# Kernel tuning notes

Measured on AMD Instinct MI355X. Metric: run time of the kernel, lower is better.

## Reference

```python
import jax, jax.numpy as jnp
import numpy as np

N = 20000
E = 320000
IN_DIM = 512
HID = 64
HEADS = 8
OUT_DIM = 40
NEG_SLOPE = 0.2


def glorot(key, shape):
    fan = shape[0] + shape[-1] if len(shape) > 1 else shape[-1]
    s = jnp.sqrt(6.0 / fan)
    return jax.random.uniform(key, shape, jnp.float32, -s, s)


def setup_inputs() -> dict:
    key = jax.random.key(0)
    ks = jax.random.split(key, 12)
    x = jax.random.normal(ks[0], (N, IN_DIM), jnp.float32)
    edge_index = jax.random.randint(ks[1], (2, E), 0, N, jnp.int64)
    return {
        "x": x,
        "edge_index": edge_index,
        "W1": glorot(ks[2], (IN_DIM, HEADS * HID)),
        "att1_src": glorot(ks[3], (HEADS, HID)),
        "att1_dst": glorot(ks[4], (HEADS, HID)),
        "b1": jnp.zeros((HEADS * HID,), jnp.float32),
        "W2": glorot(ks[5], (HEADS * HID, HEADS * HID)),
        "att2_src": glorot(ks[6], (HEADS, HID)),
        "att2_dst": glorot(ks[7], (HEADS, HID)),
        "b2": jnp.zeros((HEADS * HID,), jnp.float32),
        "W3": glorot(ks[8], (HEADS * HID, OUT_DIM)),
        "att3_src": glorot(ks[9], (1, OUT_DIM)),
        "att3_dst": glorot(ks[10], (1, OUT_DIM)),
        "b3": jnp.zeros((OUT_DIM,), jnp.float32),
    }


def gat_conv(x, src, dst, W, att_src, att_dst, bias, heads, out_c):
    # h: [N, H, C] transformed node features
    h = (x @ W).reshape(N, heads, out_c)
    a_src = jnp.sum(h * att_src, axis=-1)  # [N, H]
    a_dst = jnp.sum(h * att_dst, axis=-1)  # [N, H]
    # edge logits (message j=src -> i=dst), softmax grouped by dst
    logits = jax.nn.leaky_relu(a_src[src] + a_dst[dst], NEG_SLOPE)  # [Etot, H]
    seg_max = jax.ops.segment_max(logits, dst, num_segments=N)
    seg_max = jnp.where(jnp.isfinite(seg_max), seg_max, 0.0)
    ex = jnp.exp(logits - seg_max[dst])
    denom = jax.ops.segment_sum(ex, dst, num_segments=N)
    alpha = ex / (denom[dst] + 1e-16)  # [Etot, H]
    msg = h[src] * alpha[:, :, None]  # [Etot, H, C]
    out = jax.ops.segment_sum(msg, dst, num_segments=N)  # [N, H, C]
    return out.reshape(N, heads * out_c) + bias


def reference(x, edge_index, W1, att1_src, att1_dst, b1,
              W2, att2_src, att2_dst, b2,
              W3, att3_src, att3_dst, b3):
    # add self loops (PyG GATConv default)
    loops = jnp.arange(N, dtype=edge_index.dtype)
    src = jnp.concatenate([edge_index[0], loops])
    dst = jnp.concatenate([edge_index[1], loops])
    # dropout layers are identity in eval mode
    h = jax.nn.elu(gat_conv(x, src, dst, W1, att1_src, att1_dst, b1, HEADS, HID))
    h = jax.nn.elu(gat_conv(h, src, dst, W2, att2_src, att2_dst, b2, HEADS, HID))
    h = gat_conv(h, src, dst, W3, att3_src, att3_dst, b3, 1, OUT_DIM)
    return jax.nn.log_softmax(h, axis=-1)
```

## Files before the change

### kernel.cpp

```cpp
#include <hip/hip_runtime.h>
#include <math.h>

#define NN 20000
#define EE 320000
#define ETOT (EE + NN)
#define NEG 0.2f

typedef unsigned short ushortT;
typedef __attribute__((ext_vector_type(8))) short short8v;
typedef __attribute__((ext_vector_type(8))) unsigned short u16x8;
typedef __attribute__((ext_vector_type(4))) float f32x4;

__device__ __forceinline__ ushortT f2b(float f){
  unsigned u = __float_as_uint(f);
  u += 0x7FFFu + ((u >> 16) & 1u);
  return (ushortT)(u >> 16);
}
__device__ __forceinline__ float b2f(ushortT b){
  return __uint_as_float(((unsigned)b) << 16);
}

__global__ void k_cvt(const float* __restrict__ in, ushortT* __restrict__ outp, int n4){
  int i = blockIdx.x*blockDim.x + threadIdx.x;
  if(i < n4){
    float4 v = *reinterpret_cast<const float4*>(in + (size_t)i*4);
    ushort4 o;
    o.x = f2b(v.x); o.y = f2b(v.y); o.z = f2b(v.z); o.w = f2b(v.w);
    *reinterpret_cast<ushort4*>(outp + (size_t)i*4) = o;
  }
}

__global__ void k_wtrans(const float* __restrict__ W, ushortT* __restrict__ Wt){
  __shared__ float t[32][33];
  int bk = blockIdx.x*32, bn = blockIdx.y*32;
  int tx = threadIdx.x & 31, ty = threadIdx.x >> 5;
  for(int r=0;r<32;r+=8)
    t[ty+r][tx] = W[(size_t)(bk+ty+r)*512 + bn+tx];
  __syncthreads();
  for(int r=0;r<32;r+=8)
    Wt[(size_t)(bn+ty+r)*512 + bk+tx] = f2b(t[tx][ty+r]);
}

__global__ void k_wtrans3(const float* __restrict__ W3, ushortT* __restrict__ Wt3p){
  int idx = blockIdx.x*blockDim.x + threadIdx.x;
  if(idx >= 64*48*8) return;
  int kslot = idx / 384;
  int rem = idx - kslot*384;
  int n = rem >> 3;
  int jj = rem & 7;
  int k = kslot*8 + jj;
  float v = (n < 40) ? W3[(size_t)k*40 + n] : 0.f;
  Wt3p[idx] = f2b(v);
}

__global__ void k_count(const int* __restrict__ edst, int* __restrict__ counts){
  int e = blockIdx.x*blockDim.x + threadIdx.x;
  if(e < ETOT){
    int d = (e < EE) ? edst[e] : (e - EE);
    atomicAdd(&counts[d], 1);
  }
}

__global__ void k_scan(const int* __restrict__ counts, int* __restrict__ rowstart){
  __shared__ int lds[1024];
  int tid = threadIdx.x;
  int base = tid*20;
  int s = 0;
  for(int j=0;j<20;j++){ int i=base+j; if(i<NN) s += counts[i]; }
  lds[tid] = s; __syncthreads();
  for(int off=1; off<1024; off<<=1){
    int v = (tid>=off) ? lds[tid-off] : 0;
    __syncthreads();
    lds[tid] += v;
    __syncthreads();
  }
  int run = lds[tid] - s;
  for(int j=0;j<20;j++){
    int i = base+j;
    if(i <= NN){
      rowstart[i] = run;
      if(i < NN) run += counts[i];
    }
  }
}

__global__ void k_fill(const int* __restrict__ esrc, const int* __restrict__ edst,
                       const int* __restrict__ rowstart,
                       int* __restrict__ cursor, int* __restrict__ srcs,
                       int* __restrict__ edsts){
  int e = blockIdx.x*blockDim.x + threadIdx.x;
  if(e < ETOT){
    int d = (e < EE) ? edst[e] : (e - EE);
    int s = (e < EE) ? esrc[e] : (e - EE);
    int pos = rowstart[d] + atomicAdd(&cursor[d], 1);
    srcs[pos] = s;
    edsts[pos] = d;
  }
}

__global__ __launch_bounds__(256) void k_gemm_bf16(
    const ushortT* __restrict__ A, const ushortT* __restrict__ Bt,
    ushortT* __restrict__ Cb, int M)
{
  const int K = 512;
  __shared__ __align__(16) ushortT As[128*32];
  __shared__ __align__(16) ushortT Bs[128*32];
  int bm = blockIdx.x*128, bn = blockIdx.y*128;
  int tid = threadIdx.x, wave = tid>>6, lane = tid&63;
  int wm = (wave>>1)*64, wn = (wave&1)*64;
  f32x4 acc[4][4] = {};

  int l4 = lane>>2;
  int s4 = lane&3;
  int src_slot = s4 ^ (l4 & 3);
  int r16 = lane&15, kg = lane>>4;

  for(int k0=0;k0<K;k0+=32){
    #pragma unroll
    for(int c=0;c<2;c++){
      int chunk = wave*2 + c;
      int arow = bm + chunk*16 + l4; if(arow > M-1) arow = M-1;
      const ushortT* ga = A + (size_t)arow*K + k0 + src_slot*8;
      __builtin_amdgcn_global_load_lds(
          (const __attribute__((address_space(1))) void*)ga,
          (__attribute__((address_space(3))) void*)(As + chunk*16*32), 16, 0, 0);
      int brow = bn + chunk*16 + l4;
      const ushortT* gb = Bt + (size_t)brow*K + k0 + src_slot*8;
      __builtin_amdgcn_global_load_lds(
          (const __attribute__((address_space(1))) void*)gb,
          (__attribute__((address_space(3))) void*)(Bs + chunk*16*32), 16, 0, 0);
    }
    asm volatile("s_waitcnt vmcnt(0)");
    __syncthreads();

    short8v a_frag[4], b_frag[4];
    #pragma unroll
    for(int i=0;i<4;i++){
      int row = wm + i*16 + r16;
      a_frag[i] = *reinterpret_cast<const short8v*>(As + row*32 + ((kg ^ (row&3))<<3));
    }
    #pragma unroll
    for(int j=0;j<4;j++){
      int row = wn + j*16 + r16;
      b_frag[j] = *reinterpret_cast<const short8v*>(Bs + row*32 + ((kg ^ (row&3))<<3));
    }
    #pragma unroll
    for(int i=0;i<4;i++)
      #pragma unroll
      for(int j=0;j<4;j++)
        acc[i][j] = __builtin_amdgcn_mfma_f32_16x16x32_bf16(a_frag[i], b_frag[j], acc[i][j], 0, 0, 0);
    __syncthreads();
  }

  #pragma unroll
  for(int i=0;i<4;i++){
    #pragma unroll
    for(int j=0;j<4;j++){
      #pragma unroll
      for(int r=0;r<4;r++){
        int row = bm + wm + i*16 + kg*4 + r;
        int col = bn + wn + j*16 + r16;
        if(row < M) Cb[(size_t)row*512 + col] = f2b(acc[i][j][r]);
      }
    }
  }
}

__global__ __launch_bounds__(256) void k_gemm3m(const ushortT* __restrict__ A,
                                                const ushortT* __restrict__ Wt3p,
                                                ushortT* __restrict__ Cb, int M){
  const int K = 512;
  __shared__ __align__(16) ushortT As[128*32];
  __shared__ __align__(16) ushortT Bs[64*48*8];
  int bm = blockIdx.x*128;
  int tid = threadIdx.x, wave = tid>>6, lane = tid&63;

  #pragma unroll
  for(int it=0; it<12; it++){
    int o = (it*256 + tid)*8;
    *reinterpret_cast<u16x8*>(Bs + o) = *reinterpret_cast<const u16x8*>(Wt3p + o);
  }

  int l4 = lane>>2, s4 = lane&3;
  int src_slot = s4 ^ (l4 & 3);
  int r16 = lane&15, kg = lane>>4;
  f32x4 acc[2][3] = {};

  for(int k0=0;k0<K;k0+=32){
    #pragma unroll
    for(int c=0;c<2;c++){
      int chunk = wave*2 + c;
      int arow = bm + chunk*16 + l4; if(arow > M-1) arow = M-1;
      const ushortT* ga = A + (size_t)arow*K + k0 + src_slot*8;
      __builtin_amdgcn_global_load_lds(
          (const __attribute__((address_space(1))) void*)ga,
          (__attribute__((address_space(3))) void*)(As + chunk*16*32), 16, 0, 0);
    }
    asm volatile("s_waitcnt vmcnt(0)");
    __syncthreads();

    short8v a_frag[2], b_frag[3];
    #pragma unroll
    for(int i=0;i<2;i++){
      int row = wave*32 + i*16 + r16;
      a_frag[i] = *reinterpret_cast<const short8v*>(As + row*32 + ((kg ^ (row&3))<<3));
    }
    int kslot = (k0>>3) + kg;
    #pragma unroll
    for(int j=0;j<3;j++){
      b_frag[j] = *reinterpret_cast<const short8v*>(Bs + kslot*384 + (j*16 + r16)*8);
    }
    #pragma unroll
    for(int i=0;i<2;i++)
      #pragma unroll
      for(int j=0;j<3;j++)
        acc[i][j] = __builtin_amdgcn_mfma_f32_16x16x32_bf16(a_frag[i], b_frag[j], acc[i][j], 0, 0, 0);
    __syncthreads();
  }

  #pragma unroll
  for(int i=0;i<2;i++){
    #pragma unroll
    for(int j=0;j<3;j++){
      #pragma unroll
      for(int r=0;r<4;r++){
        int row = bm + wave*32 + i*16 + kg*4 + r;
        int col = j*16 + r16;
        if(row < M && col < 40) Cb[(size_t)row*40 + col] = f2b(acc[i][j][r]);
      }
    }
  }
}

__global__ void k_attn8(const ushortT* __restrict__ feat, const float* __restrict__ atts,
                        const float* __restrict__ attd, float* __restrict__ a_s,
                        float* __restrict__ a_d){
  int n = blockIdx.x*4 + (threadIdx.x>>6);
  int lane = threadIdx.x & 63;
  if(n >= NN) return;
  int c0 = lane*8;
  u16x8 v = *reinterpret_cast<const u16x8*>(feat + (size_t)n*512 + c0);
  float s1 = 0.f, s2 = 0.f;
  #pragma unroll
  for(int j=0;j<8;j++){
    float f = b2f((ushortT)v[j]);
    s1 += f*atts[c0+j];
    s2 += f*attd[c0+j];
  }
  #pragma unroll
  for(int off=1; off<8; off<<=1){
    s1 += __shfl_xor(s1, off);
    s2 += __shfl_xor(s2, off);
  }
  if((lane&7) == 0){
    int head = lane>>3;
    a_s[n*8+head] = s1;
    a_d[n*8+head] = s2;
  }
}

__global__ void k_attn1b(const ushortT* __restrict__ feat, const float* __restrict__ atts,
                         const float* __restrict__ attd, float* __restrict__ a_s,
                         float* __restrict__ a_d){
  int n = blockIdx.x*4 + (threadIdx.x>>6);
  int lane = threadIdx.x & 63;
  if(n >= NN) return;
  float s1 = 0.f, s2 = 0.f;
  if(lane < 40){
    float v = b2f(feat[(size_t)n*40 + lane]);
    s1 = v*atts[lane];
    s2 = v*attd[lane];
  }
  for(int off=32; off; off>>=1){
    s1 += __shfl_xor(s1, off);
    s2 += __shfl_xor(s2, off);
  }
  if(lane == 0){ a_s[n] = s1; a_d[n] = s2; }
}

__global__ void k_edge_pre(const int* __restrict__ srcs, const int* __restrict__ edsts,
                           const float* __restrict__ a_s, const float* __restrict__ a_d,
                           unsigned* __restrict__ rec){
  int pos = blockIdx.x*blockDim.x + threadIdx.x;
  if(pos >= ETOT) return;
  int s = srcs[pos], d = edsts[pos];
  float4 s0 = *reinterpret_cast<const float4*>(a_s + ((size_t)s<<3));
  float4 s1 = *reinterpret_cast<const float4*>(a_s + ((size_t)s<<3) + 4);
  float4 d0 = *reinterpret_cast<const float4*>(a_d + ((size_t)d<<3));
  float4 d1 = *reinterpret_cast<const float4*>(a_d + ((size_t)d<<3) + 4);
  float l[8] = { s0.x+d0.x, s0.y+d0.y, s0.z+d0.z, s0.w+d0.w,
                 s1.x+d1.x, s1.y+d1.y, s1.z+d1.z, s1.w+d1.w };
  unsigned sh = ((unsigned)s) << 16;
  #pragma unroll
  for(int h=0;h<8;h++){
    float al = __expf(fmaxf(l[h], NEG*l[h]));
    rec[(size_t)h*ETOT + pos] = sh | (unsigned)f2b(al);
  }
}

__global__ __launch_bounds__(512) void k_agg512(const ushortT* __restrict__ feat,
    const unsigned* __restrict__ rec, const int* __restrict__ rowstart,
    const float* __restrict__ bias, ushortT* __restrict__ outb){
  int slice = blockIdx.x & 7;
  int lane  = threadIdx.x & 63;
  int ds = lane>>3, cg = lane&7;
  int d = (blockIdx.x>>3)*64 + (int)(threadIdx.x>>6)*8 + ds;
  bool dok = d < NN;
  int p  = dok ? rowstart[d]   : 0;
  int p1 = dok ? rowstart[d+1] : 0;
  const unsigned* plane = rec + (size_t)slice*ETOT;
  unsigned cbase = ((unsigned)slice<<6) + ((unsigned)cg<<3);
  float acc[8] = {0.f,0.f,0.f,0.f,0.f,0.f,0.f,0.f};
  float dsum = 0.f;

  for(; p+4 <= p1; p += 4){
    unsigned r0 = plane[p];
    unsigned r1 = plane[p+1];
    unsigned r2 = plane[p+2];
    unsigned r3 = plane[p+3];
    u16x8 v0 = *reinterpret_cast<const u16x8*>(feat + ((r0>>16<<9) + cbase));
    u16x8 v1 = *reinterpret_cast<const u16x8*>(feat + ((r1>>16<<9) + cbase));
    u16x8 v2 = *reinterpret_cast<const u16x8*>(feat + ((r2>>16<<9) + cbase));
    u16x8 v3 = *reinterpret_cast<const u16x8*>(feat + ((r3>>16<<9) + cbase));
    float al0 = b2f((ushortT)(r0 & 0xffffu));
    float al1 = b2f((ushortT)(r1 & 0xffffu));
    float al2 = b2f((ushortT)(r2 & 0xffffu));
    float al3 = b2f((ushortT)(r3 & 0xffffu));
    dsum += al0 + al1 + al2 + al3;
    #pragma unroll
    for(int j=0;j<8;j++) acc[j] += al0*b2f((ushortT)v0[j]);
    #pragma unroll
    for(int j=0;j<8;j++) acc[j] += al1*b2f((ushortT)v1[j]);
    #pragma unroll
    for(int j=0;j<8;j++) acc[j] += al2*b2f((ushortT)v2[j]);
    #pragma unroll
    for(int j=0;j<8;j++) acc[j] += al3*b2f((ushortT)v3[j]);
  }
  while(__any(p < p1)){
    bool valid = p < p1;
    int pc = valid ? p : 0;
    unsigned r = plane[pc];
    float al = valid ? b2f((ushortT)(r & 0xffffu)) : 0.f;
    u16x8 v = *reinterpret_cast<const u16x8*>(feat + ((r>>16<<9) + cbase));
    dsum += al;
    #pragma unroll
    for(int j=0;j<8;j++) acc[j] += al*b2f((ushortT)v[j]);
    p++;
  }

  if(dok){
    float invd = 1.f/(dsum + 1e-16f);
    u16x8 ov;
    #pragma unroll
    for(int j=0;j<8;j++){
      float o = acc[j]*invd + bias[cbase+j];
      o = (o > 0.f) ? o : (__expf(o) - 1.f);
      ov[j] = f2b(o);
    }
    *reinterpret_cast<u16x8*>(outb + (size_t)d*512 + cbase) = ov;
  }
}

__global__ void k_agg_l3(const ushortT* __restrict__ feat,
    const float* __restrict__ a_s, const float* __restrict__ a_d,
    const int* __restrict__ rowstart, const int* __restrict__ srcs,
    const float* __restrict__ bias, float* __restrict__ outp){
  int d = blockIdx.x;
  int lane = threadIdx.x;
  bool act = lane < 40;
  int li = act ? lane : 0;
  float ad_v = a_d[d];
  float acc = 0.f, dsum = 0.f;
  int p0 = rowstart[d], p1 = rowstart[d+1];
  int p = p0;
  for(; p+4 <= p1; p += 4){
    int s0_ = srcs[p], s1_ = srcs[p+1], s2_ = srcs[p+2], s3_ = srcs[p+3];
    float l0 = a_s[s0_] + ad_v, l1 = a_s[s1_] + ad_v;
    float l2 = a_s[s2_] + ad_v, l3 = a_s[s3_] + ad_v;
    float v0 = b2f(feat[(size_t)s0_*40 + li]);
    float v1 = b2f(feat[(size_t)s1_*40 + li]);
    float v2 = b2f(feat[(size_t)s2_*40 + li]);
    float v3 = b2f(feat[(size_t)s3_*40 + li]);
    float al0 = __expf(fmaxf(l0, NEG*l0));
    float al1 = __expf(fmaxf(l1, NEG*l1));
    float al2 = __expf(fmaxf(l2, NEG*l2));
    float al3 = __expf(fmaxf(l3, NEG*l3));
    dsum += al0 + al1 + al2 + al3;
    acc += al0*v0 + al1*v1 + al2*v2 + al3*v3;
  }
  for(; p<p1; p++){
    int s_ = srcs[p];
    float l = a_s[s_] + ad_v;
    float al = __expf(fmaxf(l, NEG*l));
    dsum += al;
    acc += al*b2f(feat[(size_t)s_*40 + li]);
  }
  float invd = 1.f/(dsum + 1e-16f);
  float o = act ? (acc*invd + bias[lane]) : -1e30f;
  float m = o;
  for(int off=32; off; off>>=1) m = fmaxf(m, __shfl_xor(m, off));
  float e_ = act ? expf(o - m) : 0.f;
  float ssum = e_;
  for(int off=32; off; off>>=1) ssum += __shfl_xor(ssum, off);
  if(act) outp[(size_t)d*40 + lane] = o - m - logf(ssum);
}

extern "C" void kernel_launch(void* const* d_in, const int* in_sizes, int n_in,
                              void* d_out, int out_size, void* d_ws, size_t ws_size,
                              hipStream_t stream){
  const float* x   = (const float*)d_in[0];
  const int*   ei  = (const int*)d_in[1];
  const int*   esrc = ei;
  const int*   edst = ei + EE;
  const float* W1  = (const float*)d_in[2];
  const float* as1 = (const float*)d_in[3];
  const float* ad1 = (const float*)d_in[4];
  const float* b1  = (const float*)d_in[5];
  const float* W2  = (const float*)d_in[6];
  const float* as2 = (const float*)d_in[7];
  const float* ad2 = (const float*)d_in[8];
  const float* b2  = (const float*)d_in[9];
  const float* W3  = (const float*)d_in[10];
  const float* as3 = (const float*)d_in[11];
  const float* ad3 = (const float*)d_in[12];
  const float* b3  = (const float*)d_in[13];
  float* out = (float*)d_out;

  char* w = (char*)d_ws;
  size_t off = 0;
  auto alloc = [&](size_t bytes)->char*{
    char* p = w + off;
    off = (off + bytes + 255) & ~(size_t)255;
    return p;
  };
  ushortT*  xb   = (ushortT*)alloc((size_t)NN*512*2);
  ushortT*  fA   = (ushortT*)alloc((size_t)NN*512*2);
  ushortT*  fB   = (ushortT*)alloc((size_t)NN*512*2);
  ushortT*  h3b  = (ushortT*)alloc((size_t)NN*40*2);
  ushortT*  Wt1  = (ushortT*)alloc((size_t)512*512*2);
  ushortT*  Wt2  = (ushortT*)alloc((size_t)512*512*2);
  ushortT*  Wt3p = (ushortT*)alloc((size_t)64*48*8*2);
  float*    a_s  = (float*)alloc((size_t)NN*8*4);
  float*    a_d  = (float*)alloc((size_t)NN*8*4);
  unsigned* rec  = (unsigned*)alloc((size_t)8*ETOT*4);
  int* rowstart  = (int*)alloc((size_t)(NN+1)*4);
  int* cursor    = (int*)alloc((size_t)NN*4);
  int* counts    = (int*)alloc((size_t)NN*4);
  int* srcs      = (int*)alloc((size_t)ETOT*4);
  int* edsts     = (int*)alloc((size_t)ETOT*4);

  k_cvt<<<(NN*512/4 + 255)/256, 256, 0, stream>>>(x, xb, NN*512/4);
  dim3 wt_grid(16, 16);
  k_wtrans<<<wt_grid, 256, 0, stream>>>(W1, Wt1);
  k_wtrans<<<wt_grid, 256, 0, stream>>>(W2, Wt2);
  k_wtrans3<<<(64*48*8 + 255)/256, 256, 0, stream>>>(W3, Wt3p);

  hipMemsetAsync(counts, 0, (size_t)NN*4, stream);
  hipMemsetAsync(cursor, 0, (size_t)NN*4, stream);
  k_count<<<(ETOT+255)/256, 256, 0, stream>>>(edst, counts);
  k_scan<<<1, 1024, 0, stream>>>(counts, rowstart);
  k_fill<<<(ETOT+255)/256, 256, 0, stream>>>(esrc, edst, rowstart, cursor, srcs, edsts);

  dim3 mgrid((NN+127)/128, 4);
  int edge_blocks = (ETOT + 255)/256;
  int agg_blocks  = ((NN + 63)/64)*8;

  k_gemm_bf16<<<mgrid, 256, 0, stream>>>(xb, Wt1, fA, NN);
  k_attn8<<<(NN+3)/4, 256, 0, stream>>>(fA, as1, ad1, a_s, a_d);
  k_edge_pre<<<edge_blocks, 256, 0, stream>>>(srcs, edsts, a_s, a_d, rec);
  k_agg512<<<agg_blocks, 512, 0, stream>>>(fA, rec, rowstart, b1, fB);

  k_gemm_bf16<<<mgrid, 256, 0, stream>>>(fB, Wt2, fA, NN);
  k_attn8<<<(NN+3)/4, 256, 0, stream>>>(fA, as2, ad2, a_s, a_d);
  k_edge_pre<<<edge_blocks, 256, 0, stream>>>(srcs, edsts, a_s, a_d, rec);
  k_agg512<<<agg_blocks, 512, 0, stream>>>(fA, rec, rowstart, b2, fB);

  k_gemm3m<<<(NN+127)/128, 256, 0, stream>>>(fB, Wt3p, h3b, NN);
  k_attn1b<<<(NN+3)/4, 256, 0, stream>>>(h3b, as3, ad3, a_s, a_d);
  k_agg_l3<<<NN, 64, 0, stream>>>(h3b, a_s, a_d, rowstart, srcs, b3, out);
}
```

Measured before the change: 240.1 us.

## Fuse prep kernels into one launch and double GEMM K-tile to 64

Merges the x conversion and the three weight transpose/convert kernels into a single launch, with block ranges selecting the role, so three kernel launches disappear. Separately, the bf16 GEMM now stages 64-wide K tiles with an 8-way XOR swizzle and runs two MFMA sub-steps per tile, which halves the number of barrier/wait iterations. LDS use doubles to 32KB per block, which may reduce occupancy.

Result: faster. 233.4 us (-2.8%).

```diff
diff --git a/kernel.cpp b/kernel.cpp
--- a/kernel.cpp
+++ b/kernel.cpp
@@ -20,37 +20,41 @@
   return __uint_as_float(((unsigned)b) << 16);
 }
 
-__global__ void k_cvt(const float* __restrict__ in, ushortT* __restrict__ outp, int n4){
-  int i = blockIdx.x*blockDim.x + threadIdx.x;
-  if(i < n4){
-    float4 v = *reinterpret_cast<const float4*>(in + (size_t)i*4);
+__global__ void k_prep(const float* __restrict__ x, ushortT* __restrict__ xb,
+                       const float* __restrict__ W1, ushortT* __restrict__ Wt1,
+                       const float* __restrict__ W2, ushortT* __restrict__ Wt2,
+                       const float* __restrict__ W3, ushortT* __restrict__ Wt3p){
+  int b = blockIdx.x;
+  if(b < 10000){
+    int i = b*256 + threadIdx.x;
+    float4 v = *reinterpret_cast<const float4*>(x + (size_t)i*4);
     ushort4 o;
     o.x = f2b(v.x); o.y = f2b(v.y); o.z = f2b(v.z); o.w = f2b(v.w);
-    *reinterpret_cast<ushort4*>(outp + (size_t)i*4) = o;
-  }
-}
-
-__global__ void k_wtrans(const float* __restrict__ W, ushortT* __restrict__ Wt){
-  __shared__ float t[32][33];
-  int bk = blockIdx.x*32, bn = blockIdx.y*32;
-  int tx = threadIdx.x & 31, ty = threadIdx.x >> 5;
-  for(int r=0;r<32;r+=8)
-    t[ty+r][tx] = W[(size_t)(bk+ty+r)*512 + bn+tx];
-  __syncthreads();
-  for(int r=0;r<32;r+=8)
-    Wt[(size_t)(bn+ty+r)*512 + bk+tx] = f2b(t[tx][ty+r]);
-}
-
-__global__ void k_wtrans3(const float* __restrict__ W3, ushortT* __restrict__ Wt3p){
-  int idx = blockIdx.x*blockDim.x + threadIdx.x;
-  if(idx >= 64*48*8) return;
-  int kslot = idx / 384;
-  int rem = idx - kslot*384;
-  int n = rem >> 3;
-  int jj = rem & 7;
-  int k = kslot*8 + jj;
-  float v = (n < 40) ? W3[(size_t)k*40 + n] : 0.f;
-  Wt3p[idx] = f2b(v);
+    *reinterpret_cast<ushort4*>(xb + (size_t)i*4) = o;
+  } else if(b < 10512){
+    const float* W = (b < 10256) ? W1 : W2;
+    ushortT* Wt    = (b < 10256) ? Wt1 : Wt2;
+    int bb = (b < 10256) ? (b - 10000) : (b - 10256);
+    __shared__ float t[32][33];
+    int bk = (bb & 15)*32, bn = (bb >> 4)*32;
+    int tx = threadIdx.x & 31, ty = threadIdx.x >> 5;
+    for(int r=0;r<32;r+=8)
+      t[ty+r][tx] = W[(size_t)(bk+ty+r)*512 + bn+tx];
+    __syncthreads();
+    for(int r=0;r<32;r+=8)
+      Wt[(size_t)(bn+ty+r)*512 + bk+tx] = f2b(t[tx][ty+r]);
+  } else {
+    int idx = (b - 10512)*256 + threadIdx.x;
+    if(idx < 64*48*8){
+      int kslot = idx / 384;
+      int rem = idx - kslot*384;
+      int n = rem >> 3;
+      int jj = rem & 7;
+      int k = kslot*8 + jj;
+      float v = (n < 40) ? W3[(size_t)k*40 + n] : 0.f;
+      Wt3p[idx] = f2b(v);
+    }
+  }
 }
 
 __global__ void k_count(const int* __restrict__ edst, int* __restrict__ counts){
@@ -103,52 +107,55 @@
     ushortT* __restrict__ Cb, int M)
 {
   const int K = 512;
-  __shared__ __align__(16) ushortT As[128*32];
-  __shared__ __align__(16) ushortT Bs[128*32];
+  __shared__ __align__(16) ushortT As[128*64];
+  __shared__ __align__(16) ushortT Bs[128*64];
   int bm = blockIdx.x*128, bn = blockIdx.y*128;
   int tid = threadIdx.x, wave = tid>>6, lane = tid&63;
   int wm = (wave>>1)*64, wn = (wave&1)*64;
   f32x4 acc[4][4] = {};
 
-  int l4 = lane>>2;
-  int s4 = lane&3;
-  int src_slot = s4 ^ (l4 & 3);
+  int l8 = lane>>3;
+  int s8 = lane&7;
+  int src_slot = s8 ^ l8;
   int r16 = lane&15, kg = lane>>4;
 
-  for(int k0=0;k0<K;k0+=32){
-    #pragma unroll
-    for(int c=0;c<2;c++){
-      int chunk = wave*2 + c;
-      int arow = bm + chunk*16 + l4; if(arow > M-1) arow = M-1;
+  for(int k0=0;k0<K;k0+=64){
+    #pragma unroll
+    for(int c=0;c<4;c++){
+      int chunk = wave*4 + c;
+      int arow = bm + chunk*8 + l8; if(arow > M-1) arow = M-1;
       const ushortT* ga = A + (size_t)arow*K + k0 + src_slot*8;
       __builtin_amdgcn_global_load_lds(
           (const __attribute__((address_space(1))) void*)ga,
-          (__attribute__((address_space(3))) void*)(As + chunk*16*32), 16, 0, 0);
-      int brow = bn + chunk*16 + l4;
+          (__attribute__((address_space(3))) void*)(As + chunk*8*64), 16, 0, 0);
+      int brow = bn + chunk*8 + l8;
       const ushortT* gb = Bt + (size_t)brow*K + k0 + src_slot*8;
       __builtin_amdgcn_global_load_lds(
           (const __attribute__((address_space(1))) void*)gb,
-          (__attribute__((address_space(3))) void*)(Bs + chunk*16*32), 16, 0, 0);
+          (__attribute__((address_space(3))) void*)(Bs + chunk*8*64), 16, 0, 0);
     }
     asm volatile("s_waitcnt vmcnt(0)");
     __syncthreads();
 
-    short8v a_frag[4], b_frag[4];
-    #pragma unroll
-    for(int i=0;i<4;i++){
-      int row = wm + i*16 + r16;
-      a_frag[i] = *reinterpret_cast<const short8v*>(As + row*32 + ((kg ^ (row&3))<<3));
-    }
-    #pragma unroll
-    for(int j=0;j<4;j++){
-      int row = wn + j*16 + r16;
-      b_frag[j] = *reinterpret_cast<const short8v*>(Bs + row*32 + ((kg ^ (row&3))<<3));
-    }
-    #pragma unroll
-    for(int i=0;i<4;i++)
-      #pragma unroll
-      for(int j=0;j<4;j++)
-        acc[i][j] = __builtin_amdgcn_mfma_f32_16x16x32_bf16(a_frag[i], b_frag[j], acc[i][j], 0, 0, 0);
+    #pragma unroll
+    for(int h=0;h<2;h++){
+      short8v a_frag[4], b_frag[4];
+      #pragma unroll
+      for(int i=0;i<4;i++){
+        int row = wm + i*16 + r16;
+        a_frag[i] = *reinterpret_cast<const short8v*>(As + row*64 + (((h*4+kg) ^ (row&7))<<3));
+      }
+      #pragma unroll
+      for(int j=0;j<4;j++){
+        int row = wn + j*16 + r16;
+        b_frag[j] = *reinterpret_cast<const short8v*>(Bs + row*64 + (((h*4+kg) ^ (row&7))<<3));
+      }
+      #pragma unroll
+      for(int i=0;i<4;i++)
+        #pragma unroll
+        for(int j=0;j<4;j++)
+          acc[i][j] = __builtin_amdgcn_mfma_f32_16x16x32_bf16(a_frag[i], b_frag[j], acc[i][j], 0, 0, 0);
+    }
     __syncthreads();
   }
 
@@ -449,11 +456,7 @@
   int* srcs      = (int*)alloc((size_t)ETOT*4);
   int* edsts     = (int*)alloc((size_t)ETOT*4);
 
-  k_cvt<<<(NN*512/4 + 255)/256, 256, 0, stream>>>(x, xb, NN*512/4);
-  dim3 wt_grid(16, 16);
-  k_wtrans<<<wt_grid, 256, 0, stream>>>(W1, Wt1);
-  k_wtrans<<<wt_grid, 256, 0, stream>>>(W2, Wt2);
-  k_wtrans3<<<(64*48*8 + 255)/256, 256, 0, stream>>>(W3, Wt3p);
+  k_prep<<<10608, 256, 0, stream>>>(x, xb, W1, Wt1, W2, Wt2, W3, Wt3p);
 
   hipMemsetAsync(counts, 0, (size_t)NN*4, stream);
   hipMemsetAsync(cursor, 0, (size_t)NN*4, stream);
```
